# Optimization experiments

Hardware: AMD Instinct MI355X
Metric: run time of the kernel (lower is better)

Reference implementation:

```python
import jax, jax.numpy as jnp
import numpy as np

B, S, H = 1, 4096, 2048
NH, NKV, HD = 16, 4, 128  # query heads, kv heads, head_dim
THETA = 1000000.0
NEG = -1e9


def setup_inputs() -> dict:
    key = jax.random.key(0)
    ks = jax.random.split(key, 5)
    hidden_states = jax.random.normal(ks[0], (B, S, H), jnp.float32) * 0.02
    Wq = jax.random.normal(ks[1], (H, NH * HD), jnp.float32) * 0.02
    Wk = jax.random.normal(ks[2], (H, NKV * HD), jnp.float32) * 0.02
    Wv = jax.random.normal(ks[3], (H, NKV * HD), jnp.float32) * 0.02
    Wo = jax.random.normal(ks[4], (H, H), jnp.float32) * 0.02
    # additive causal mask [B,1,S,S]
    causal = jnp.tril(jnp.ones((S, S), bool))
    attention_mask = jnp.where(causal, 0.0, NEG).astype(jnp.float32)[None, None]
    position_ids = jnp.arange(S, dtype=jnp.int32)[None]
    return dict(hidden_states=hidden_states, Wq=Wq, Wk=Wk, Wv=Wv, Wo=Wo,
                attention_mask=attention_mask, position_ids=position_ids)


def _rotate_half(x):
    return jnp.concatenate([-x[..., HD // 2:], x[..., :HD // 2]], axis=-1)


def reference(hidden_states, Wq, Wk, Wv, Wo, attention_mask, position_ids):
    # projections -> [B, heads, S, HD]
    q = (hidden_states @ Wq).reshape(B, S, NH, HD).transpose(0, 2, 1, 3)
    k = (hidden_states @ Wk).reshape(B, S, NKV, HD).transpose(0, 2, 1, 3)
    v = (hidden_states @ Wv).reshape(B, S, NKV, HD).transpose(0, 2, 1, 3)

    # RoPE (HF style: freqs duplicated across halves, rotate_half)
    inv_freq = 1.0 / (THETA ** (jnp.arange(0, HD, 2, dtype=jnp.float32) / HD))
    freqs = position_ids.astype(jnp.float32)[..., None] * inv_freq  # [B,S,HD/2]
    emb = jnp.concatenate([freqs, freqs], axis=-1)                  # [B,S,HD]
    cos = jnp.cos(emb)[:, None].astype(q.dtype)                     # [B,1,S,HD]
    sin = jnp.sin(emb)[:, None].astype(q.dtype)
    q = q * cos + _rotate_half(q) * sin
    k = k * cos + _rotate_half(k) * sin

    # GQA: repeat each kv head consecutively (matches torch repeat_kv)
    rep = NH // NKV
    k = jnp.repeat(k, rep, axis=1)
    v = jnp.repeat(v, rep, axis=1)

    scale = 1.0 / jnp.sqrt(jnp.float32(HD))
    scores = jnp.einsum('bhqd,bhkd->bhqk', q, k) * scale + attention_mask
    attn = jax.nn.softmax(scores.astype(jnp.float32), axis=-1).astype(q.dtype)
    out = jnp.einsum('bhqk,bhkd->bhqd', attn, v)  # [B,NH,S,HD]
    out = out.transpose(0, 2, 1, 3).reshape(B, S, H)
    return out @ Wo
```

## Files before the change

### kernel.cpp

```cpp
#include <hip/hip_runtime.h>
#include <stdint.h>

typedef uint16_t u16;
typedef __bf16  bf16x8 __attribute__((ext_vector_type(8)));
typedef float   f32x4  __attribute__((ext_vector_type(4)));
typedef uint16_t u16x8 __attribute__((ext_vector_type(8), may_alias));

typedef const __attribute__((address_space(1))) void* gas_p;
typedef __attribute__((address_space(3))) void* las_p;

__device__ __forceinline__ void load_lds16(const void* g, void* l) {
    __builtin_amdgcn_global_load_lds((gas_p)g, (las_p)l, 16, 0, 0);
}

__device__ __forceinline__ u16 f2bf(float f) {
    uint32_t u = __builtin_bit_cast(uint32_t, f);
    u += 0x7FFFu + ((u >> 16) & 1u);
    return (u16)(u >> 16);
}
__device__ __forceinline__ float bf2f(u16 h) {
    uint32_t u = ((uint32_t)h) << 16;
    return __builtin_bit_cast(float, u);
}
__device__ __forceinline__ bf16x8 ld_frag(const u16* p) {
    u16x8 t = *(const u16x8*)p;
    return __builtin_bit_cast(bf16x8, t);
}

__global__ __launch_bounds__(256) void convert_hidden(const float* __restrict__ in,
                                                      u16* __restrict__ out, int n8) {
    int i = blockIdx.x * 256 + threadIdx.x;
    if (i >= n8) return;
    const float* p = in + (size_t)i * 8;
    u16x8 o;
#pragma unroll
    for (int j = 0; j < 8; j++) o[j] = f2bf(p[j]);
    *(u16x8*)(out + (size_t)i * 8) = o;
}

__global__ __launch_bounds__(256) void transpose_cvt(const float* __restrict__ in,
                                                     u16* __restrict__ out,
                                                     int R, int C) {
    __shared__ u16 tile[64][65];
    const int tx = threadIdx.x;
    const int bc = blockIdx.x * 64;
    const int br = blockIdx.y * 64;
#pragma unroll
    for (int i = 0; i < 16; i++) {
        int idx = tx + i * 256;
        int r = idx >> 6, c = idx & 63;
        tile[r][c] = f2bf(in[(size_t)(br + r) * C + bc + c]);
    }
    __syncthreads();
#pragma unroll
    for (int i = 0; i < 16; i++) {
        int idx = tx + i * 256;
        int r = idx >> 6, c = idx & 63;
        out[(size_t)(bc + r) * R + br + c] = tile[c][r];
    }
}

__global__ __launch_bounds__(256) void transpose_b16(const u16* __restrict__ in,
                                                     u16* __restrict__ out,
                                                     int R, int C, int ldin, int off) {
    __shared__ u16 tile[64][65];
    const int tx = threadIdx.x;
    const int bc = blockIdx.x * 64;
    const int br = blockIdx.y * 64;
#pragma unroll
    for (int i = 0; i < 16; i++) {
        int idx = tx + i * 256;
        int r = idx >> 6, c = idx & 63;
        tile[r][c] = in[(size_t)(br + r) * ldin + off + bc + c];
    }
    __syncthreads();
#pragma unroll
    for (int i = 0; i < 16; i++) {
        int idx = tx + i * 256;
        int r = idx >> 6, c = idx & 63;
        out[(size_t)(bc + r) * R + br + c] = tile[c][r];
    }
}

#define TM 128
#define TN 128
#define TK 32

__global__ __launch_bounds__(256) void gemm_qkv(const u16* __restrict__ A,
                                                const u16* __restrict__ WqT,
                                                const u16* __restrict__ WkvT,
                                                u16* __restrict__ Qb,
                                                u16* __restrict__ KVb) {
    __shared__ u16 As[TM * TK];
    __shared__ u16 Bs[TN * TK];
    const int K = 2048;
    const int tid  = threadIdx.x;
    const int wave = tid >> 6;
    const int lane = tid & 63;
    const int l15  = lane & 15;
    const int quad = lane >> 4;
    const int m0 = blockIdx.y * TM;
    const int n0 = blockIdx.x * TN;
    const u16* Bt;
    u16* C;
    int ldC, cbase;
    if (n0 < 2048) { Bt = WqT + (size_t)n0 * K;          C = Qb;  ldC = 2048; cbase = n0; }
    else           { Bt = WkvT + (size_t)(n0 - 2048) * K; C = KVb; ldC = 1024; cbase = n0 - 2048; }
    const int wm = (wave >> 1) * 64;
    const int wn = (wave & 1) * 64;

    f32x4 acc[4][4] = {};

    const int srow = tid >> 2;
    const int scol = (tid & 3) * 8;
    const u16* Ap0 = A  + (size_t)(m0 + srow) * K + scol;
    const u16* Ap1 = A  + (size_t)(m0 + 64 + srow) * K + scol;
    const u16* Bp0 = Bt + (size_t)srow * K + scol;
    const u16* Bp1 = Bt + (size_t)(64 + srow) * K + scol;
    u16* AsD0 = As + wave * 512;
    u16* AsD1 = As + 2048 + wave * 512;
    u16* BsD0 = Bs + wave * 512;
    u16* BsD1 = Bs + 2048 + wave * 512;

    for (int k0 = 0; k0 < K; k0 += TK) {
        load_lds16(Ap0 + k0, AsD0);
        load_lds16(Ap1 + k0, AsD1);
        load_lds16(Bp0 + k0, BsD0);
        load_lds16(Bp1 + k0, BsD1);
        __syncthreads();
        bf16x8 af[4], bfr[4];
#pragma unroll
        for (int i = 0; i < 4; i++)
            af[i] = ld_frag(&As[(wm + i * 16 + l15) * TK + quad * 8]);
#pragma unroll
        for (int j = 0; j < 4; j++)
            bfr[j] = ld_frag(&Bs[(wn + j * 16 + l15) * TK + quad * 8]);
#pragma unroll
        for (int i = 0; i < 4; i++)
#pragma unroll
            for (int j = 0; j < 4; j++)
                acc[i][j] = __builtin_amdgcn_mfma_f32_16x16x32_bf16(af[i], bfr[j], acc[i][j], 0, 0, 0);
        __syncthreads();
    }
#pragma unroll
    for (int i = 0; i < 4; i++)
#pragma unroll
        for (int j = 0; j < 4; j++)
#pragma unroll
            for (int r = 0; r < 4; r++) {
                int row = m0 + wm + i * 16 + quad * 4 + r;
                int col = cbase + wn + j * 16 + l15;
                C[(size_t)row * ldC + col] = f2bf(acc[i][j][r]);
            }
}

template <bool F32OUT>
__global__ __launch_bounds__(256) void gemm_bt(const u16* __restrict__ A,
                                               const u16* __restrict__ Bt,
                                               void* __restrict__ Cp,
                                               int M, int N, int K) {
    __shared__ u16 As[TM * TK];
    __shared__ u16 Bs[TN * TK];
    const int tid  = threadIdx.x;
    const int wave = tid >> 6;
    const int lane = tid & 63;
    const int l15  = lane & 15;
    const int quad = lane >> 4;
    const int m0 = blockIdx.y * TM;
    const int n0 = blockIdx.x * TN;
    const int wm = (wave >> 1) * 64;
    const int wn = (wave & 1) * 64;

    f32x4 acc[4][4] = {};

    const int srow = tid >> 2;
    const int scol = (tid & 3) * 8;
    const u16* Ap0 = A  + (size_t)(m0 + srow) * K + scol;
    const u16* Ap1 = A  + (size_t)(m0 + 64 + srow) * K + scol;
    const u16* Bp0 = Bt + (size_t)(n0 + srow) * K + scol;
    const u16* Bp1 = Bt + (size_t)(n0 + 64 + srow) * K + scol;
    u16* AsD0 = As + wave * 512;
    u16* AsD1 = As + 2048 + wave * 512;
    u16* BsD0 = Bs + wave * 512;
    u16* BsD1 = Bs + 2048 + wave * 512;

    for (int k0 = 0; k0 < K; k0 += TK) {
        load_lds16(Ap0 + k0, AsD0);
        load_lds16(Ap1 + k0, AsD1);
        load_lds16(Bp0 + k0, BsD0);
        load_lds16(Bp1 + k0, BsD1);
        __syncthreads();
        bf16x8 af[4], bfr[4];
#pragma unroll
        for (int i = 0; i < 4; i++)
            af[i] = ld_frag(&As[(wm + i * 16 + l15) * TK + quad * 8]);
#pragma unroll
        for (int j = 0; j < 4; j++)
            bfr[j] = ld_frag(&Bs[(wn + j * 16 + l15) * TK + quad * 8]);
#pragma unroll
        for (int i = 0; i < 4; i++)
#pragma unroll
            for (int j = 0; j < 4; j++)
                acc[i][j] = __builtin_amdgcn_mfma_f32_16x16x32_bf16(af[i], bfr[j], acc[i][j], 0, 0, 0);
        __syncthreads();
    }
#pragma unroll
    for (int i = 0; i < 4; i++)
#pragma unroll
        for (int j = 0; j < 4; j++)
#pragma unroll
            for (int r = 0; r < 4; r++) {
                int row = m0 + wm + i * 16 + quad * 4 + r;
                int col = n0 + wn + j * 16 + l15;
                if (F32OUT)
                    ((float*)Cp)[(size_t)row * N + col] = acc[i][j][r];
                else
                    ((u16*)Cp)[(size_t)row * N + col] = f2bf(acc[i][j][r]);
            }
}

__global__ __launch_bounds__(256) void rope_kernel(u16* __restrict__ Q,
                                                   u16* __restrict__ KV) {
    int g = blockIdx.x * 256 + threadIdx.x;
    int d = g & 63;
    int row = g >> 6;
    int s = row / 20;
    int hh = row - s * 20;
    u16* buf = (hh < 16) ? (Q + (size_t)s * 2048 + hh * 128)
                         : (KV + (size_t)s * 1024 + (hh - 16) * 128);
    float p = (float)s;
    float angle = p * exp2f((float)d * (-19.931568569324174f / 64.0f));
    float c = cosf(angle), sn = sinf(angle);
    float x0 = bf2f(buf[d]), x1 = bf2f(buf[d + 64]);
    buf[d]      = f2bf(x0 * c - x1 * sn);
    buf[d + 64] = f2bf(x1 * c + x0 * sn);
}

#define SCALE2 0.1275430214486847f
#define PSTR 40

__global__ __launch_bounds__(256, 2) void flash_attn3(const u16* __restrict__ Q,
                                                      const u16* __restrict__ KVb,
                                                      const u16* __restrict__ VT,
                                                      u16* __restrict__ O) {
    __shared__ u16 Ks[8192];
    __shared__ u16 Vs[8192];
    __shared__ u16 Plds[4][2 * 16 * PSTR];
    const int tid  = threadIdx.x;
    const int wave = tid >> 6;
    const int lane = tid & 63;
    const int l15  = lane & 15;
    const int quad = lane >> 4;
    const int bx   = blockIdx.x;
    const int h    = blockIdx.y;
    const int kvh  = h >> 2;
    const int q_lo = bx * 64;
    const int q_hi = (63 - bx) * 64;

    bf16x8 qlo[4], qhi[4];
    {
        const u16* plo = Q + (size_t)(q_lo + wave * 16 + l15) * 2048 + h * 128 + quad * 8;
        const u16* phi = Q + (size_t)(q_hi + wave * 16 + l15) * 2048 + h * 128 + quad * 8;
#pragma unroll
        for (int s4 = 0; s4 < 4; s4++) { qlo[s4] = ld_frag(plo + s4 * 32); qhi[s4] = ld_frag(phi + s4 * 32); }
    }

    f32x4 acc_lo[8] = {}, acc_hi[8] = {};
    float l_lo[4] = {}, l_hi[4] = {};
    const int qt_lo = q_lo + wave * 16;
    const int qt_hi = q_hi + wave * 16;
    const int qrow_lo = qt_lo + quad * 4;
    const int qrow_hi = qt_hi + quad * 4;

    const u16* srcK[4];
    const u16* srcV[4];
#pragma unroll
    for (int r = 0; r < 4; r++) {
        int p = r * 256 + tid;
        int kv = p >> 4;
        srcK[r] = KVb + (size_t)kv * 1024 + kvh * 128 + ((((p & 15) - kv) & 15) * 8);
        int d = p >> 3;
        srcV[r] = VT + (size_t)(kvh * 128 + d) * 4096 + ((((p & 7) - (d & 7)) & 7) * 8);
    }
    u16* PW = &Plds[wave][0];

    const int nkv = 64 - bx;
    const int nlo = bx + 1;

    for (int kvb = 0; kvb < nkv; kvb++) {
        const int kv0 = kvb * 64;
        __syncthreads();
#pragma unroll
        for (int r = 0; r < 4; r++) {
            load_lds16(srcK[r] + (size_t)kv0 * 1024, Ks + r * 2048 + wave * 512);
            load_lds16(srcV[r] + kv0, Vs + r * 2048 + wave * 512);
        }
        __syncthreads();

        const bool do_lo = (kvb < nlo);
        f32x4 svl[4] = {}, svh[4] = {};
#pragma unroll
        for (int s4 = 0; s4 < 4; s4++)
#pragma unroll
            for (int t = 0; t < 4; t++) {
                int row = t * 16 + l15;
                bf16x8 kf = ld_frag(&Ks[row * 128 + (((s4 * 4 + quad) + row) & 15) * 8]);
                svh[t] = __builtin_amdgcn_mfma_f32_16x16x32_bf16(qhi[s4], kf, svh[t], 0, 0, 0);
                if (do_lo)
                    svl[t] = __builtin_amdgcn_mfma_f32_16x16x32_bf16(qlo[s4], kf, svl[t], 0, 0, 0);
            }

#pragma unroll
        for (int tile = 0; tile < 2; tile++) {
            if (tile == 0 && !do_lo) continue;
            const f32x4* sv = (tile == 0) ? svl : svh;
            float* l_i      = (tile == 0) ? l_lo : l_hi;
            f32x4* acc      = (tile == 0) ? acc_lo : acc_hi;
            const int qrow0 = (tile == 0) ? qrow_lo : qrow_hi;

            float pv[4][4];
#pragma unroll
            for (int r = 0; r < 4; r++) {
                int qrow = qrow0 + r;
                float rs = 0.f;
#pragma unroll
                for (int t = 0; t < 4; t++) {
                    float p = exp2f(sv[t][r] * SCALE2);
                    if (kv0 + t * 16 + l15 > qrow) p = 0.f;
                    pv[t][r] = p;
                    rs += p;
                }
#pragma unroll
                for (int off = 1; off < 16; off <<= 1)
                    rs += __shfl_xor(rs, off, 64);
                l_i[r] += rs;
            }
#pragma unroll
            for (int t = 0; t < 2; t++)
#pragma unroll
                for (int r = 0; r < 4; r++)
                    PW[(quad * 4 + r) * PSTR + t * 16 + l15] = f2bf(pv[t][r]);
#pragma unroll
            for (int t = 0; t < 2; t++)
#pragma unroll
                for (int r = 0; r < 4; r++)
                    PW[16 * PSTR + (quad * 4 + r) * PSTR + t * 16 + l15] = f2bf(pv[2 + t][r]);
            bf16x8 pf0 = ld_frag(&PW[l15 * PSTR + quad * 8]);
            bf16x8 pf1 = ld_frag(&PW[16 * PSTR + l15 * PSTR + quad * 8]);
#pragma unroll
            for (int nt = 0; nt < 8; nt++) {
                int row = nt * 16 + l15;
                bf16x8 vf0 = ld_frag(&Vs[row * 64 + ((quad + (row & 7)) & 7) * 8]);
                bf16x8 vf1 = ld_frag(&Vs[row * 64 + (((4 + quad) + (row & 7)) & 7) * 8]);
                acc[nt] = __builtin_amdgcn_mfma_f32_16x16x32_bf16(pf0, vf0, acc[nt], 0, 0, 0);
                acc[nt] = __builtin_amdgcn_mfma_f32_16x16x32_bf16(pf1, vf1, acc[nt], 0, 0, 0);
            }
        }
    }

#pragma unroll
    for (int r = 0; r < 4; r++) {
        float invl = 1.0f / l_lo[r];
        float invh = 1.0f / l_hi[r];
        int rowl = qrow_lo + r, rowh = qrow_hi + r;
#pragma unroll
        for (int nt = 0; nt < 8; nt++) {
            O[(size_t)rowl * 2048 + h * 128 + nt * 16 + l15] = f2bf(acc_lo[nt][r] * invl);
            O[(size_t)rowh * 2048 + h * 128 + nt * 16 + l15] = f2bf(acc_hi[nt][r] * invh);
        }
    }
}

extern "C" void kernel_launch(void* const* d_in, const int* in_sizes, int n_in,
                              void* d_out, int out_size, void* d_ws, size_t ws_size,
                              hipStream_t stream) {
    const float* hidden = (const float*)d_in[0];
    const float* Wq = (const float*)d_in[1];
    const float* Wk = (const float*)d_in[2];
    const float* Wv = (const float*)d_in[3];
    const float* Wo = (const float*)d_in[4];
    float* out = (float*)d_out;

    u16* ws   = (u16*)d_ws;
    u16* Hb   = ws;
    u16* Qb   = Hb   + 8388608;
    u16* KVb  = Qb   + 8388608;
    u16* WqT  = KVb  + 4194304;
    u16* WkvT = WqT  + 4194304;
    u16* VT   = WkvT + 2097152;

    convert_hidden<<<4096, 256, 0, stream>>>(hidden, Hb, 1048576);

    transpose_cvt<<<dim3(32, 32), 256, 0, stream>>>(Wq, WqT, 2048, 2048);
    transpose_cvt<<<dim3(8, 32), 256, 0, stream>>>(Wk, WkvT, 2048, 512);
    transpose_cvt<<<dim3(8, 32), 256, 0, stream>>>(Wv, WkvT + 1048576, 2048, 512);

    gemm_qkv<<<dim3(24, 32), 256, 0, stream>>>(Hb, WqT, WkvT, Qb, KVb);

    u16* WoT = WqT;
    transpose_cvt<<<dim3(32, 32), 256, 0, stream>>>(Wo, WoT, 2048, 2048);

    rope_kernel<<<dim3(20480), 256, 0, stream>>>(Qb, KVb);

    transpose_b16<<<dim3(8, 64), 256, 0, stream>>>(KVb, VT, 4096, 512, 1024, 512);

    u16* Ob = Hb;
    flash_attn3<<<dim3(32, 16), 256, 0, stream>>>(Qb, KVb, VT, Ob);

    gemm_bt<true><<<dim3(16, 32), 256, 0, stream>>>(Ob, WoT, out, 4096, 2048, 2048);
}
```

Measured before the change: 467.8 us.

## Fuse RoPE into QKV GEMM, double-buffer KV in attention, merge weight transposes

Several changes land together. RoPE is now applied in the QKV GEMM epilogue, with the wave column mapping remapped so each rotation pair sits in one wave's registers, which removes the separate rope kernel and its read and write of Q/K. The attention kernel double-buffers K/V tiles in LDS with a single barrier per iteration, prefolds the softmax scale into Q, and applies the causal mask only on diagonal blocks. The three weight transposes are merged into one launch. The costs are doubled LDS for K/V, which may affect occupancy, and an extra bf16 rounding of the scaled Q.

```diff
diff --git a/kernel.cpp b/kernel.cpp
--- a/kernel.cpp
+++ b/kernel.cpp
@@ -36,6 +36,38 @@
 #pragma unroll
     for (int j = 0; j < 8; j++) o[j] = f2bf(p[j]);
     *(u16x8*)(out + (size_t)i * 8) = o;
+}
+
+__global__ __launch_bounds__(256) void transpose_w3(const float* __restrict__ Wq,
+                                                    const float* __restrict__ Wk,
+                                                    const float* __restrict__ Wv,
+                                                    u16* __restrict__ WqT,
+                                                    u16* __restrict__ WkvT) {
+    __shared__ u16 tile[64][65];
+    const int z = blockIdx.z;
+    const float* in;
+    u16* out;
+    int C;
+    if (z == 0)      { in = Wq; out = WqT;            C = 2048; }
+    else if (z == 1) { in = Wk; out = WkvT;           C = 512; if (blockIdx.x >= 8) return; }
+    else             { in = Wv; out = WkvT + 1048576; C = 512; if (blockIdx.x >= 8) return; }
+    const int R = 2048;
+    const int tx = threadIdx.x;
+    const int bc = blockIdx.x * 64;
+    const int br = blockIdx.y * 64;
+#pragma unroll
+    for (int i = 0; i < 16; i++) {
+        int idx = tx + i * 256;
+        int r = idx >> 6, c = idx & 63;
+        tile[r][c] = f2bf(in[(size_t)(br + r) * C + bc + c]);
+    }
+    __syncthreads();
+#pragma unroll
+    for (int i = 0; i < 16; i++) {
+        int idx = tx + i * 256;
+        int r = idx >> 6, c = idx & 63;
+        out[(size_t)(bc + r) * R + br + c] = tile[c][r];
+    }
 }
 
 __global__ __launch_bounds__(256) void transpose_cvt(const float* __restrict__ in,
@@ -104,10 +136,13 @@
     const u16* Bt;
     u16* C;
     int ldC, cbase;
-    if (n0 < 2048) { Bt = WqT + (size_t)n0 * K;          C = Qb;  ldC = 2048; cbase = n0; }
+    if (n0 < 2048) { Bt = WqT + (size_t)n0 * K;           C = Qb;  ldC = 2048; cbase = n0; }
     else           { Bt = WkvT + (size_t)(n0 - 2048) * K; C = KVb; ldC = 1024; cbase = n0 - 2048; }
     const int wm = (wave >> 1) * 64;
-    const int wn = (wave & 1) * 64;
+    const int w1 = wave & 1;
+    int cbx[4];
+    cbx[0] = 2 * w1;     cbx[1] = 2 * w1 + 1;
+    cbx[2] = 2 * w1 + 4; cbx[3] = 2 * w1 + 5;
 
     f32x4 acc[4][4] = {};
 
@@ -134,7 +169,7 @@
             af[i] = ld_frag(&As[(wm + i * 16 + l15) * TK + quad * 8]);
 #pragma unroll
         for (int j = 0; j < 4; j++)
-            bfr[j] = ld_frag(&Bs[(wn + j * 16 + l15) * TK + quad * 8]);
+            bfr[j] = ld_frag(&Bs[(cbx[j] * 16 + l15) * TK + quad * 8]);
 #pragma unroll
         for (int i = 0; i < 4; i++)
 #pragma unroll
@@ -142,6 +177,31 @@
                 acc[i][j] = __builtin_amdgcn_mfma_f32_16x16x32_bf16(af[i], bfr[j], acc[i][j], 0, 0, 0);
         __syncthreads();
     }
+
+    const bool dorope = (n0 < 2048) || (cbase < 512);
+    if (dorope) {
+        float inv0 = exp2f((float)(cbx[0] * 16 + l15) * (-19.931568569324174f / 64.0f));
+        float inv1 = exp2f((float)(cbx[1] * 16 + l15) * (-19.931568569324174f / 64.0f));
+#pragma unroll
+        for (int i = 0; i < 4; i++)
+#pragma unroll
+            for (int r = 0; r < 4; r++) {
+                float pos = (float)(m0 + wm + i * 16 + quad * 4 + r);
+                {
+                    float ang = pos * inv0, sn = sinf(ang), cs = cosf(ang);
+                    float x0 = acc[i][0][r], x1 = acc[i][2][r];
+                    acc[i][0][r] = x0 * cs - x1 * sn;
+                    acc[i][2][r] = x1 * cs + x0 * sn;
+                }
+                {
+                    float ang = pos * inv1, sn = sinf(ang), cs = cosf(ang);
+                    float x0 = acc[i][1][r], x1 = acc[i][3][r];
+                    acc[i][1][r] = x0 * cs - x1 * sn;
+                    acc[i][3][r] = x1 * cs + x0 * sn;
+                }
+            }
+    }
+
 #pragma unroll
     for (int i = 0; i < 4; i++)
 #pragma unroll
@@ -149,7 +209,7 @@
 #pragma unroll
             for (int r = 0; r < 4; r++) {
                 int row = m0 + wm + i * 16 + quad * 4 + r;
-                int col = cbase + wn + j * 16 + l15;
+                int col = cbase + cbx[j] * 16 + l15;
                 C[(size_t)row * ldC + col] = f2bf(acc[i][j][r]);
             }
 }
@@ -219,32 +279,54 @@
             }
 }
 
-__global__ __launch_bounds__(256) void rope_kernel(u16* __restrict__ Q,
-                                                   u16* __restrict__ KV) {
-    int g = blockIdx.x * 256 + threadIdx.x;
-    int d = g & 63;
-    int row = g >> 6;
-    int s = row / 20;
-    int hh = row - s * 20;
-    u16* buf = (hh < 16) ? (Q + (size_t)s * 2048 + hh * 128)
-                         : (KV + (size_t)s * 1024 + (hh - 16) * 128);
-    float p = (float)s;
-    float angle = p * exp2f((float)d * (-19.931568569324174f / 64.0f));
-    float c = cosf(angle), sn = sinf(angle);
-    float x0 = bf2f(buf[d]), x1 = bf2f(buf[d + 64]);
-    buf[d]      = f2bf(x0 * c - x1 * sn);
-    buf[d + 64] = f2bf(x1 * c + x0 * sn);
-}
-
 #define SCALE2 0.1275430214486847f
 #define PSTR 40
 
-__global__ __launch_bounds__(256, 2) void flash_attn3(const u16* __restrict__ Q,
+__device__ __forceinline__ void fa_tile(const f32x4* sv, float* l_i, f32x4* acc,
+                                        u16* PW, const u16* VsC, int kv0, int qrow0,
+                                        int l15, int quad, bool domask) {
+    float pv[4][4];
+#pragma unroll
+    for (int r = 0; r < 4; r++) {
+        int qrow = qrow0 + r;
+        float rs = 0.f;
+#pragma unroll
+        for (int t = 0; t < 4; t++) {
+            float p = exp2f(sv[t][r]);
+            if (domask && (kv0 + t * 16 + l15 > qrow)) p = 0.f;
+            pv[t][r] = p;
+            rs += p;
+        }
+#pragma unroll
+        for (int off = 1; off < 16; off <<= 1)
+            rs += __shfl_xor(rs, off, 64);
+        l_i[r] += rs;
+    }
+#pragma unroll
+    for (int t = 0; t < 2; t++)
+#pragma unroll
+        for (int r = 0; r < 4; r++) {
+            PW[(quad * 4 + r) * PSTR + t * 16 + l15] = f2bf(pv[t][r]);
+            PW[16 * PSTR + (quad * 4 + r) * PSTR + t * 16 + l15] = f2bf(pv[2 + t][r]);
+        }
+    bf16x8 pf0 = ld_frag(&PW[l15 * PSTR + quad * 8]);
+    bf16x8 pf1 = ld_frag(&PW[16 * PSTR + l15 * PSTR + quad * 8]);
+#pragma unroll
+    for (int nt = 0; nt < 8; nt++) {
+        int row = nt * 16 + l15;
+        bf16x8 vf0 = ld_frag(&VsC[row * 64 + ((quad + (row & 7)) & 7) * 8]);
+        bf16x8 vf1 = ld_frag(&VsC[row * 64 + (((4 + quad) + (row & 7)) & 7) * 8]);
+        acc[nt] = __builtin_amdgcn_mfma_f32_16x16x32_bf16(pf0, vf0, acc[nt], 0, 0, 0);
+        acc[nt] = __builtin_amdgcn_mfma_f32_16x16x32_bf16(pf1, vf1, acc[nt], 0, 0, 0);
+    }
+}
+
+__global__ __launch_bounds__(256, 2) void flash_attn4(const u16* __restrict__ Q,
                                                       const u16* __restrict__ KVb,
                                                       const u16* __restrict__ VT,
                                                       u16* __restrict__ O) {
-    __shared__ u16 Ks[8192];
-    __shared__ u16 Vs[8192];
+    __shared__ u16 Ks[2][8192];
+    __shared__ u16 Vs[2][8192];
     __shared__ u16 Plds[4][2 * 16 * PSTR];
     const int tid  = threadIdx.x;
     const int wave = tid >> 6;
@@ -262,15 +344,24 @@
         const u16* plo = Q + (size_t)(q_lo + wave * 16 + l15) * 2048 + h * 128 + quad * 8;
         const u16* phi = Q + (size_t)(q_hi + wave * 16 + l15) * 2048 + h * 128 + quad * 8;
 #pragma unroll
-        for (int s4 = 0; s4 < 4; s4++) { qlo[s4] = ld_frag(plo + s4 * 32); qhi[s4] = ld_frag(phi + s4 * 32); }
+        for (int s4 = 0; s4 < 4; s4++) {
+            u16x8 a = *(const u16x8*)(plo + s4 * 32);
+            u16x8 b = *(const u16x8*)(phi + s4 * 32);
+            u16x8 as, bs;
+#pragma unroll
+            for (int j = 0; j < 8; j++) {
+                as[j] = f2bf(bf2f(a[j]) * SCALE2);
+                bs[j] = f2bf(bf2f(b[j]) * SCALE2);
+            }
+            qlo[s4] = __builtin_bit_cast(bf16x8, as);
+            qhi[s4] = __builtin_bit_cast(bf16x8, bs);
+        }
     }
 
     f32x4 acc_lo[8] = {}, acc_hi[8] = {};
     float l_lo[4] = {}, l_hi[4] = {};
-    const int qt_lo = q_lo + wave * 16;
-    const int qt_hi = q_hi + wave * 16;
-    const int qrow_lo = qt_lo + quad * 4;
-    const int qrow_hi = qt_hi + quad * 4;
+    const int qrow_lo = q_lo + wave * 16 + quad * 4;
+    const int qrow_hi = q_hi + wave * 16 + quad * 4;
 
     const u16* srcK[4];
     const u16* srcV[4];
@@ -287,15 +378,26 @@
     const int nkv = 64 - bx;
     const int nlo = bx + 1;
 
+#pragma unroll
+    for (int r = 0; r < 4; r++) {
+        load_lds16(srcK[r], &Ks[0][r * 2048 + wave * 512]);
+        load_lds16(srcV[r], &Vs[0][r * 2048 + wave * 512]);
+    }
+    __syncthreads();
+
     for (int kvb = 0; kvb < nkv; kvb++) {
         const int kv0 = kvb * 64;
-        __syncthreads();
-#pragma unroll
-        for (int r = 0; r < 4; r++) {
-            load_lds16(srcK[r] + (size_t)kv0 * 1024, Ks + r * 2048 + wave * 512);
-            load_lds16(srcV[r] + kv0, Vs + r * 2048 + wave * 512);
+        const int cur = kvb & 1;
+        if (kvb + 1 < nkv) {
+            const int kvn = (kvb + 1) * 64;
+#pragma unroll
+            for (int r = 0; r < 4; r++) {
+                load_lds16(srcK[r] + (size_t)kvn * 1024, &Ks[cur ^ 1][r * 2048 + wave * 512]);
+                load_lds16(srcV[r] + kvn, &Vs[cur ^ 1][r * 2048 + wave * 512]);
+            }
         }
-        __syncthreads();
+        const u16* KsC = &Ks[cur][0];
+        const u16* VsC = &Vs[cur][0];
 
         const bool do_lo = (kvb < nlo);
         f32x4 svl[4] = {}, svh[4] = {};
@@ -304,58 +406,17 @@
 #pragma unroll
             for (int t = 0; t < 4; t++) {
                 int row = t * 16 + l15;
-                bf16x8 kf = ld_frag(&Ks[row * 128 + (((s4 * 4 + quad) + row) & 15) * 8]);
+                bf16x8 kf = ld_frag(&KsC[row * 128 + (((s4 * 4 + quad) + row) & 15) * 8]);
                 svh[t] = __builtin_amdgcn_mfma_f32_16x16x32_bf16(qhi[s4], kf, svh[t], 0, 0, 0);
                 if (do_lo)
                     svl[t] = __builtin_amdgcn_mfma_f32_16x16x32_bf16(qlo[s4], kf, svl[t], 0, 0, 0);
             }
 
-#pragma unroll
-        for (int tile = 0; tile < 2; tile++) {
-            if (tile == 0 && !do_lo) continue;
-            const f32x4* sv = (tile == 0) ? svl : svh;
-            float* l_i      = (tile == 0) ? l_lo : l_hi;
-            f32x4* acc      = (tile == 0) ? acc_lo : acc_hi;
-            const int qrow0 = (tile == 0) ? qrow_lo : qrow_hi;
-
-            float pv[4][4];
-#pragma unroll
-            for (int r = 0; r < 4; r++) {
-                int qrow = qrow0 + r;
-                float rs = 0.f;
-#pragma unroll
-                for (int t = 0; t < 4; t++) {
-                    float p = exp2f(sv[t][r] * SCALE2);
-                    if (kv0 + t * 16 + l15 > qrow) p = 0.f;
-                    pv[t][r] = p;
-                    rs += p;
-                }
-#pragma unroll
-                for (int off = 1; off < 16; off <<= 1)
-                    rs += __shfl_xor(rs, off, 64);
-                l_i[r] += rs;
-            }
-#pragma unroll
-            for (int t = 0; t < 2; t++)
-#pragma unroll
-                for (int r = 0; r < 4; r++)
-                    PW[(quad * 4 + r) * PSTR + t * 16 + l15] = f2bf(pv[t][r]);
-#pragma unroll
-            for (int t = 0; t < 2; t++)
-#pragma unroll
-                for (int r = 0; r < 4; r++)
-                    PW[16 * PSTR + (quad * 4 + r) * PSTR + t * 16 + l15] = f2bf(pv[2 + t][r]);
-            bf16x8 pf0 = ld_frag(&PW[l15 * PSTR + quad * 8]);
-            bf16x8 pf1 = ld_frag(&PW[16 * PSTR + l15 * PSTR + quad * 8]);
-#pragma unroll
-            for (int nt = 0; nt < 8; nt++) {
-                int row = nt * 16 + l15;
-                bf16x8 vf0 = ld_frag(&Vs[row * 64 + ((quad + (row & 7)) & 7) * 8]);
-                bf16x8 vf1 = ld_frag(&Vs[row * 64 + (((4 + quad) + (row & 7)) & 7) * 8]);
-                acc[nt] = __builtin_amdgcn_mfma_f32_16x16x32_bf16(pf0, vf0, acc[nt], 0, 0, 0);
-                acc[nt] = __builtin_amdgcn_mfma_f32_16x16x32_bf16(pf1, vf1, acc[nt], 0, 0, 0);
-            }
-        }
+        if (do_lo)
+            fa_tile(svl, l_lo, acc_lo, PW, VsC, kv0, qrow_lo, l15, quad, kvb == nlo - 1);
+        fa_tile(svh, l_hi, acc_hi, PW, VsC, kv0, qrow_hi, l15, quad, kvb == nkv - 1);
+
+        __syncthreads();
     }
 
 #pragma unroll
@@ -391,21 +452,17 @@
 
     convert_hidden<<<4096, 256, 0, stream>>>(hidden, Hb, 1048576);
 
-    transpose_cvt<<<dim3(32, 32), 256, 0, stream>>>(Wq, WqT, 2048, 2048);
-    transpose_cvt<<<dim3(8, 32), 256, 0, stream>>>(Wk, WkvT, 2048, 512);
-    transpose_cvt<<<dim3(8, 32), 256, 0, stream>>>(Wv, WkvT + 1048576, 2048, 512);
+    transpose_w3<<<dim3(32, 32, 3), 256, 0, stream>>>(Wq, Wk, Wv, WqT, WkvT);
 
     gemm_qkv<<<dim3(24, 32), 256, 0, stream>>>(Hb, WqT, WkvT, Qb, KVb);
 
     u16* WoT = WqT;
     transpose_cvt<<<dim3(32, 32), 256, 0, stream>>>(Wo, WoT, 2048, 2048);
 
-    rope_kernel<<<dim3(20480), 256, 0, stream>>>(Qb, KVb);
-
     transpose_b16<<<dim3(8, 64), 256, 0, stream>>>(KVb, VT, 4096, 512, 1024, 512);
 
     u16* Ob = Hb;
-    flash_attn3<<<dim3(32, 16), 256, 0, stream>>>(Qb, KVb, VT, Ob);
+    flash_attn4<<<dim3(32, 16), 256, 0, stream>>>(Qb, KVb, VT, Ob);
 
     gemm_bt<true><<<dim3(16, 32), 256, 0, stream>>>(Ob, WoT, out, 4096, 2048, 2048);
 }
```

Measured after the change: 1.154 ms. 147% more time.
